# Kernel tuning notes

Hardware: AMD Instinct MI355X
Metric: run time of the kernel (lower is better)

The kernel has to match this reference:

```python
import jax, jax.numpy as jnp
import numpy as np


def setup_inputs() -> dict:
    key = jax.random.key(0)
    kq, kk, kv = jax.random.split(key, 3)
    B, H, S, D = 2, 16, 2048, 64
    Q = jax.random.normal(kq, (B, H, S, D), dtype=jnp.float32)
    K = jax.random.normal(kk, (B, H, S, D), dtype=jnp.float32)
    V = jax.random.normal(kv, (B, H, S, D), dtype=jnp.float32)
    return {"Q": Q, "K": K, "V": V}


def reference(Q, K, V):
    # Faithful to the torch module: NO 1/sqrt(d_k) scaling (d_k is computed
    # but never used in the original forward).
    scores = jnp.einsum('bhqd,bhkd->bhqk', Q, K)      # [B,H,S,S]
    attn = jax.nn.softmax(scores, axis=-1)
    out = jnp.einsum('bhqk,bhkd->bhqd', attn, V)      # [B,H,S,D]
    return out
```

## Files before the change

kernel.cpp:

```cpp
#include <hip/hip_runtime.h>


typedef __bf16    bf16_t;
typedef _Float16  f16_t;
typedef __bf16    bf16x8 __attribute__((ext_vector_type(8)));
typedef _Float16  f16x8  __attribute__((ext_vector_type(8)));
typedef float     f32x4  __attribute__((ext_vector_type(4)));

constexpr int S  = 2048;
constexpr int Dh = 64;
constexpr int KT = 64;
constexpr int QT = 128;
constexpr float LOG2E = 1.44269504088896340736f;

__device__ __forceinline__ int sw(int row, int col) {
    return row * 64 + ((((col >> 3) ^ (row & 7)) << 3) | (col & 7));
}

__device__ __forceinline__ int swp(int row, int k) {
    return sw(row >> 1, (row & 1) * 32 + k);
}

template<int SN>
__global__ __launch_bounds__(256, 4)
void attn_kernel(const float* __restrict__ Qg,
                 const float* __restrict__ Kg,
                 const float* __restrict__ Vg,
                 float* __restrict__ Og,
                 float* __restrict__ Opart,
                 float* __restrict__ lpart)
{
    __shared__ alignas(16) f16_t  Khs[KT * Dh];
    __shared__ alignas(16) bf16_t Vts[Dh * KT];
    __shared__ alignas(16) bf16_t Pbs[64 * 64];

    const int tid  = threadIdx.x;
    const int lane = tid & 63;
    const int wv   = tid >> 6;
    const int l15  = lane & 15;
    const int qd   = lane >> 4;
    const int wb   = wv * 32;

    const int bx   = blockIdx.x;
    const int head = bx & 31;
    const int r5   = bx >> 5;
    const int qt   = r5 / SN;
    const int half = r5 % SN;
    const int tile = head * 16 + qt;
    const int ch0  = (SN == 3) ? half * 11 : half * 16;
    const int nch  = (SN == 3) ? (half == 2 ? 10 : 11) : (SN == 2 ? 16 : 32);

    const float* Qp = Qg + (size_t)tile * QT * Dh;
    const float* Kp = Kg + (size_t)head * S * Dh;
    const float* Vp = Vg + (size_t)head * S * Dh;

    const int skey = tid >> 4;
    const int sc4  = (tid & 15) * 4;
    const int vkb  = (tid >> 4) * 4;
    const int vc4  = (tid & 15) * 4;

    f16x8 qf[2][2];
    #pragma unroll
    for (int sub = 0; sub < 2; ++sub) {
        const float* qrow = Qp + (size_t)(wb + sub * 16 + l15) * Dh;
        #pragma unroll
        for (int ks = 0; ks < 2; ++ks) {
            const float* p = qrow + ks * 32 + qd * 8;
            const float4 a = *(const float4*)(p);
            const float4 b = *(const float4*)(p + 4);
            const float xs[8] = {a.x, a.y, a.z, a.w, b.x, b.y, b.z, b.w};
            #pragma unroll
            for (int j = 0; j < 8; ++j) qf[sub][ks][j] = (f16_t)(xs[j] * LOG2E);
        }
    }

    f32x4 oa[2][4];
    float lp[2];
    #pragma unroll
    for (int s2 = 0; s2 < 2; ++s2) {
        lp[s2] = 0.f;
        #pragma unroll
        for (int t = 0; t < 4; ++t) oa[s2][t] = (f32x4){0.f, 0.f, 0.f, 0.f};
    }

    float4 kbuf[4], vbuf[4];
    {
        const float* Kc = Kp + (size_t)ch0 * KT * Dh;
        const float* Vc = Vp + (size_t)ch0 * KT * Dh;
        #pragma unroll
        for (int it = 0; it < 4; ++it)
            kbuf[it] = *(const float4*)(Kc + (size_t)(it * 16 + skey) * Dh + sc4);
        #pragma unroll
        for (int i = 0; i < 4; ++i)
            vbuf[i] = *(const float4*)(Vc + (size_t)(vkb + i) * Dh + vc4);
    }

    #pragma unroll 1
    for (int ci = 0; ci < nch; ++ci) {
        __syncthreads();

        #pragma unroll
        for (int it = 0; it < 4; ++it) {
            const float xs[4] = {kbuf[it].x, kbuf[it].y, kbuf[it].z, kbuf[it].w};
            union { f16_t h[4]; uint2 u; } ph;
            #pragma unroll
            for (int j = 0; j < 4; ++j) ph.h[j] = (f16_t)xs[j];
            *(uint2*)&Khs[sw(it * 16 + skey, sc4)] = ph.u;
        }
        {
            const float rs[4][4] = {{vbuf[0].x, vbuf[1].x, vbuf[2].x, vbuf[3].x},
                                    {vbuf[0].y, vbuf[1].y, vbuf[2].y, vbuf[3].y},
                                    {vbuf[0].z, vbuf[1].z, vbuf[2].z, vbuf[3].z},
                                    {vbuf[0].w, vbuf[1].w, vbuf[2].w, vbuf[3].w}};
            #pragma unroll
            for (int i = 0; i < 4; ++i) {
                union { bf16_t h[4]; uint2 u; } pv;
                #pragma unroll
                for (int j = 0; j < 4; ++j) pv.h[j] = (bf16_t)rs[i][j];
                *(uint2*)&Vts[sw(vc4 + i, vkb)] = pv.u;
            }
        }
        __syncthreads();

        if (ci + 1 < nch) {
            const float* Kc = Kp + (size_t)(ch0 + ci + 1) * KT * Dh;
            const float* Vc = Vp + (size_t)(ch0 + ci + 1) * KT * Dh;
            #pragma unroll
            for (int it = 0; it < 4; ++it)
                kbuf[it] = *(const float4*)(Kc + (size_t)(it * 16 + skey) * Dh + sc4);
            #pragma unroll
            for (int i = 0; i < 4; ++i)
                vbuf[i] = *(const float4*)(Vc + (size_t)(vkb + i) * Dh + vc4);
        }

        #pragma unroll
        for (int np = 0; np < 2; ++np) {
            f32x4 st[2][2];
            #pragma unroll
            for (int s2 = 0; s2 < 2; ++s2)
                #pragma unroll
                for (int t = 0; t < 2; ++t) st[s2][t] = (f32x4){0.f, 0.f, 0.f, 0.f};
            __builtin_amdgcn_s_setprio(1);
            #pragma unroll
            for (int ks = 0; ks < 2; ++ks) {
                const int co = ks * 32 + qd * 8;
                const f16x8 ak0 = *(const f16x8*)&Khs[sw((np * 2 + 0) * 16 + l15, co)];
                const f16x8 ak1 = *(const f16x8*)&Khs[sw((np * 2 + 1) * 16 + l15, co)];
                #pragma unroll
                for (int s2 = 0; s2 < 2; ++s2) {
                    st[s2][0] = __builtin_amdgcn_mfma_f32_16x16x32_f16(ak0, qf[s2][ks], st[s2][0], 0, 0, 0);
                    st[s2][1] = __builtin_amdgcn_mfma_f32_16x16x32_f16(ak1, qf[s2][ks], st[s2][1], 0, 0, 0);
                }
            }
            __builtin_amdgcn_s_setprio(0);
            #pragma unroll
            for (int s2 = 0; s2 < 2; ++s2) {
                #pragma unroll
                for (int t = 0; t < 2; ++t) {
                    union { bf16_t h[4]; uint2 u; } pb;
                    #pragma unroll
                    for (int r = 0; r < 4; ++r) {
                        const float e = __builtin_amdgcn_exp2f(st[s2][t][r]);
                        lp[s2] += e;
                        pb.h[r] = (bf16_t)e;
                    }
                    *(uint2*)&Pbs[swp(wb + s2 * 16 + l15, t * 16 + qd * 4)] = pb.u;
                }
            }
            const int co = np * 32 + qd * 8;
            const bf16x8 pa0 = *(const bf16x8*)&Pbs[swp(wb + l15,      qd * 8)];
            const bf16x8 pa1 = *(const bf16x8*)&Pbs[swp(wb + 16 + l15, qd * 8)];
            __builtin_amdgcn_s_setprio(1);
            #pragma unroll
            for (int dt = 0; dt < 4; ++dt) {
                const bf16x8 vb = *(const bf16x8*)&Vts[sw(dt * 16 + l15, co)];
                oa[0][dt] = __builtin_amdgcn_mfma_f32_16x16x32_bf16(pa0, vb, oa[0][dt], 0, 0, 0);
                oa[1][dt] = __builtin_amdgcn_mfma_f32_16x16x32_bf16(pa1, vb, oa[1][dt], 0, 0, 0);
            }
            __builtin_amdgcn_s_setprio(0);
        }
    }

    #pragma unroll
    for (int s2 = 0; s2 < 2; ++s2) {
        lp[s2] += __shfl_xor(lp[s2], 16, 64);
        lp[s2] += __shfl_xor(lp[s2], 32, 64);
    }

    if (SN > 1) {
        float* Po = Opart + (size_t)(tile * SN + half) * (QT * Dh);
        float* lq = lpart + (size_t)(tile * SN + half) * QT;
        #pragma unroll
        for (int s2 = 0; s2 < 2; ++s2) {
            if (qd == 0) lq[wb + s2 * 16 + l15] = lp[s2];
            #pragma unroll
            for (int r = 0; r < 4; ++r) {
                const int row = wb + s2 * 16 + qd * 4 + r;
                #pragma unroll
                for (int dt = 0; dt < 4; ++dt)
                    Po[(size_t)row * Dh + dt * 16 + l15] = oa[s2][dt][r];
            }
        }
    } else {
        float* Op = Og + (size_t)tile * QT * Dh;
        #pragma unroll
        for (int s2 = 0; s2 < 2; ++s2) {
            #pragma unroll
            for (int r = 0; r < 4; ++r) {
                const float inv = 1.0f / __shfl(lp[s2], qd * 4 + r, 64);
                const int row = wb + s2 * 16 + qd * 4 + r;
                #pragma unroll
                for (int dt = 0; dt < 4; ++dt)
                    Op[(size_t)row * Dh + dt * 16 + l15] = oa[s2][dt][r] * inv;
            }
        }
    }
}

template<int SN>
__global__ __launch_bounds__(256)
void combine_kernel(const float* __restrict__ Opart,
                    const float* __restrict__ lpart,
                    float* __restrict__ Og)
{
    const int i  = blockIdx.x * 256 + threadIdx.x;
    const int q  = i >> 11;
    const int rw = (i >> 4) & 127;
    const size_t e = (size_t)(i & 2047) * 4;
    float4 acc = {0.f, 0.f, 0.f, 0.f};
    float  l   = 0.f;
    #pragma unroll
    for (int h = 0; h < SN; ++h) {
        const float4 a = *(const float4*)(Opart + (size_t)(q * SN + h) * (QT * Dh) + e);
        l += lpart[(size_t)(q * SN + h) * QT + rw];
        acc.x += a.x; acc.y += a.y; acc.z += a.z; acc.w += a.w;
    }
    const float inv = 1.0f / l;
    float4 o;
    o.x = acc.x * inv; o.y = acc.y * inv; o.z = acc.z * inv; o.w = acc.w * inv;
    *(float4*)(Og + (size_t)i * 4) = o;
}

extern "C" void kernel_launch(void* const* d_in, const int* in_sizes, int n_in,
                              void* d_out, int out_size, void* d_ws, size_t ws_size,
                              hipStream_t stream)
{
    const float* Q = (const float*)d_in[0];
    const float* K = (const float*)d_in[1];
    const float* V = (const float*)d_in[2];
    float*       O = (float*)d_out;

    constexpr size_t TILE_O = (size_t)QT * Dh;
    constexpr size_t NEED3  = (512ull * 3 * (TILE_O + QT)) * sizeof(float);
    constexpr size_t NEED2  = (512ull * 2 * (TILE_O + QT)) * sizeof(float);
    const int n4 = (int)(512 * TILE_O / 4);

    if (ws_size >= NEED3) {
        float* Opart = (float*)d_ws;
        float* lpart = Opart + 512ull * 3 * TILE_O;
        attn_kernel<3><<<dim3(1536), dim3(256), 0, stream>>>(
            Q, K, V, nullptr, Opart, lpart);
        combine_kernel<3><<<dim3(n4 / 256), dim3(256), 0, stream>>>(Opart, lpart, O);
    } else if (ws_size >= NEED2) {
        float* Opart = (float*)d_ws;
        float* lpart = Opart + 512ull * 2 * TILE_O;
        attn_kernel<2><<<dim3(1024), dim3(256), 0, stream>>>(
            Q, K, V, nullptr, Opart, lpart);
        combine_kernel<2><<<dim3(n4 / 256), dim3(256), 0, stream>>>(Opart, lpart, O);
    } else {
        attn_kernel<1><<<dim3(512), dim3(256), 0, stream>>>(
            Q, K, V, O, nullptr, nullptr);
    }
}
```

Baseline: 143.4 us.

## Double-buffer K/V shared tiles to drop one barrier per chunk

```diff
diff --git a/kernel.cpp b/kernel.cpp
--- a/kernel.cpp
+++ b/kernel.cpp
@@ -30,8 +30,8 @@
                  float* __restrict__ Opart,
                  float* __restrict__ lpart)
 {
-    __shared__ alignas(16) f16_t  Khs[KT * Dh];
-    __shared__ alignas(16) bf16_t Vts[Dh * KT];
+    __shared__ alignas(16) f16_t  Khs[2][KT * Dh];
+    __shared__ alignas(16) bf16_t Vts[2][KT * Dh];
     __shared__ alignas(16) bf16_t Pbs[64 * 64];
 
     const int tid  = threadIdx.x;
@@ -84,54 +84,47 @@
     }
 
     float4 kbuf[4], vbuf[4];
-    {
-        const float* Kc = Kp + (size_t)ch0 * KT * Dh;
-        const float* Vc = Vp + (size_t)ch0 * KT * Dh;
+
+    auto LOADCH = [&](int c) {
+        const float* Kc = Kp + (size_t)c * KT * Dh;
+        const float* Vc = Vp + (size_t)c * KT * Dh;
         #pragma unroll
         for (int it = 0; it < 4; ++it)
             kbuf[it] = *(const float4*)(Kc + (size_t)(it * 16 + skey) * Dh + sc4);
         #pragma unroll
         for (int i = 0; i < 4; ++i)
             vbuf[i] = *(const float4*)(Vc + (size_t)(vkb + i) * Dh + vc4);
-    }
-
-    #pragma unroll 1
-    for (int ci = 0; ci < nch; ++ci) {
-        __syncthreads();
-
+    };
+    auto WRITEBUF = [&](int b) {
         #pragma unroll
         for (int it = 0; it < 4; ++it) {
             const float xs[4] = {kbuf[it].x, kbuf[it].y, kbuf[it].z, kbuf[it].w};
             union { f16_t h[4]; uint2 u; } ph;
             #pragma unroll
             for (int j = 0; j < 4; ++j) ph.h[j] = (f16_t)xs[j];
-            *(uint2*)&Khs[sw(it * 16 + skey, sc4)] = ph.u;
-        }
-        {
-            const float rs[4][4] = {{vbuf[0].x, vbuf[1].x, vbuf[2].x, vbuf[3].x},
-                                    {vbuf[0].y, vbuf[1].y, vbuf[2].y, vbuf[3].y},
-                                    {vbuf[0].z, vbuf[1].z, vbuf[2].z, vbuf[3].z},
-                                    {vbuf[0].w, vbuf[1].w, vbuf[2].w, vbuf[3].w}};
-            #pragma unroll
-            for (int i = 0; i < 4; ++i) {
-                union { bf16_t h[4]; uint2 u; } pv;
-                #pragma unroll
-                for (int j = 0; j < 4; ++j) pv.h[j] = (bf16_t)rs[i][j];
-                *(uint2*)&Vts[sw(vc4 + i, vkb)] = pv.u;
-            }
-        }
-        __syncthreads();
-
-        if (ci + 1 < nch) {
-            const float* Kc = Kp + (size_t)(ch0 + ci + 1) * KT * Dh;
-            const float* Vc = Vp + (size_t)(ch0 + ci + 1) * KT * Dh;
-            #pragma unroll
-            for (int it = 0; it < 4; ++it)
-                kbuf[it] = *(const float4*)(Kc + (size_t)(it * 16 + skey) * Dh + sc4);
-            #pragma unroll
-            for (int i = 0; i < 4; ++i)
-                vbuf[i] = *(const float4*)(Vc + (size_t)(vkb + i) * Dh + vc4);
-        }
+            *(uint2*)&Khs[b][sw(it * 16 + skey, sc4)] = ph.u;
+        }
+        const float rs[4][4] = {{vbuf[0].x, vbuf[1].x, vbuf[2].x, vbuf[3].x},
+                                {vbuf[0].y, vbuf[1].y, vbuf[2].y, vbuf[3].y},
+                                {vbuf[0].z, vbuf[1].z, vbuf[2].z, vbuf[3].z},
+                                {vbuf[0].w, vbuf[1].w, vbuf[2].w, vbuf[3].w}};
+        #pragma unroll
+        for (int i = 0; i < 4; ++i) {
+            union { bf16_t h[4]; uint2 u; } pv;
+            #pragma unroll
+            for (int j = 0; j < 4; ++j) pv.h[j] = (bf16_t)rs[i][j];
+            *(uint2*)&Vts[b][sw(vc4 + i, vkb)] = pv.u;
+        }
+    };
+
+    LOADCH(ch0);
+    WRITEBUF(0);
+    if (nch > 1) LOADCH(ch0 + 1);
+    __syncthreads();
+
+    #pragma unroll 1
+    for (int ci = 0; ci < nch; ++ci) {
+        const int cur = ci & 1;
 
         #pragma unroll
         for (int np = 0; np < 2; ++np) {
@@ -144,8 +137,8 @@
             #pragma unroll
             for (int ks = 0; ks < 2; ++ks) {
                 const int co = ks * 32 + qd * 8;
-                const f16x8 ak0 = *(const f16x8*)&Khs[sw((np * 2 + 0) * 16 + l15, co)];
-                const f16x8 ak1 = *(const f16x8*)&Khs[sw((np * 2 + 1) * 16 + l15, co)];
+                const f16x8 ak0 = *(const f16x8*)&Khs[cur][sw((np * 2 + 0) * 16 + l15, co)];
+                const f16x8 ak1 = *(const f16x8*)&Khs[cur][sw((np * 2 + 1) * 16 + l15, co)];
                 #pragma unroll
                 for (int s2 = 0; s2 < 2; ++s2) {
                     st[s2][0] = __builtin_amdgcn_mfma_f32_16x16x32_f16(ak0, qf[s2][ks], st[s2][0], 0, 0, 0);
@@ -173,11 +166,17 @@
             __builtin_amdgcn_s_setprio(1);
             #pragma unroll
             for (int dt = 0; dt < 4; ++dt) {
-                const bf16x8 vb = *(const bf16x8*)&Vts[sw(dt * 16 + l15, co)];
+                const bf16x8 vb = *(const bf16x8*)&Vts[cur][sw(dt * 16 + l15, co)];
                 oa[0][dt] = __builtin_amdgcn_mfma_f32_16x16x32_bf16(pa0, vb, oa[0][dt], 0, 0, 0);
                 oa[1][dt] = __builtin_amdgcn_mfma_f32_16x16x32_bf16(pa1, vb, oa[1][dt], 0, 0, 0);
             }
             __builtin_amdgcn_s_setprio(0);
+        }
+
+        if (ci + 1 < nch) {
+            WRITEBUF(cur ^ 1);
+            if (ci + 2 < nch) LOADCH(ch0 + ci + 2);
+            __syncthreads();
         }
     }
 
```

New measurement: 201.3 us. 1.4x slower.
